# Optimization experiments

Hardware: AMD Instinct MI355X
Metric: run time of the kernel (lower is better)

Reference implementation:

```python
import jax, jax.numpy as jnp
import numpy as np
from jax import lax

D_MODEL, N_STATE, L_LEN = 1024, 64, 4096
DT_INIT = 0.1


def hippo_legs_matrix(N):
    # Standard HiPPO-LegS: A[n,k] = -sqrt(2n+1)sqrt(2k+1) if n>k, -(n+1) if n==k, 0 else
    n = np.arange(N, dtype=np.float32)
    r = np.sqrt(2.0 * n + 1.0)
    A = np.where(n[:, None] > n[None, :], r[:, None] * r[None, :], 0.0)
    A = -(A + np.diag(n + 1.0))
    B = r.copy()
    return jnp.asarray(A, jnp.float32), jnp.asarray(B, jnp.float32)


def setup_inputs() -> dict:
    key = jax.random.key(0)
    kB, kC = jax.random.split(key)
    A_ct, B_ref = hippo_legs_matrix(N_STATE)
    B0 = jnp.tile(B_ref[None, :], (D_MODEL, 1))
    B = B0 + 0.01 * jax.random.normal(kB, (D_MODEL, N_STATE), jnp.float32)
    C = jax.random.normal(kC, (D_MODEL, N_STATE), jnp.float32) * 0.1
    D = jnp.zeros((D_MODEL,), jnp.float32)
    log_dt = jnp.asarray(np.log(DT_INIT), jnp.float32)
    return {"A_ct": A_ct, "B": B, "C": C, "D": D, "log_dt": log_dt}


def reference(A_ct, B, C, D, log_dt):
    dt = jnp.exp(log_dt)
    N = A_ct.shape[0]
    I = jnp.eye(N, dtype=A_ct.dtype)
    M = I - (dt / 2.0) * A_ct          # (N,N)
    P = I + (dt / 2.0) * A_ct          # (N,N)
    A_bar = jnp.linalg.solve(M, P)     # (N,N)
    # B_bar[d] = M^{-1} (dt * B[d])  -> solve on transposed batch
    B_bar = jnp.linalg.solve(M, (dt * B).T).T  # (D,N)

    def step(x, _):
        # x: (D,N) state; emit readout then advance
        y = jnp.sum(C * x, axis=-1)    # (D,)
        return x @ A_bar.T, y

    _, ys = lax.scan(step, B_bar, None, length=L_LEN)  # ys: (L,D)
    K = ys.T                                           # (D,L)
    K = K.at[:, 0].add(D)
    return K[:, None, :]                                # (D,1,L)
```

## Files before the change

### kernel.cpp

```cpp
#include <hip/hip_runtime.h>
#include <math.h>


#define BPAD 72
#define ARR (64 * BPAD)

#define WS_BBAR   16
#define WS_SPL    65552
#define WS_MV     (WS_SPL + 12*8192)
#define WS_GT     (WS_MV + 4096)
#define WS_H      (WS_GT + 64*4096)
#define WS_W      (WS_H + 64*4096)
#define WS_X      (WS_W + 1024*4096)

using bf16x8 = __attribute__((ext_vector_type(8))) short;
using f32x4v = __attribute__((ext_vector_type(4))) float;
typedef unsigned short ushort_t;

__device__ __forceinline__ ushort_t f2bf(float x) {
  unsigned u = __builtin_bit_cast(unsigned, x);
  return (ushort_t)((u + 0x7FFFu + ((u >> 16) & 1u)) >> 16);
}
__device__ __forceinline__ float bfhi(float x) {
  unsigned u = __builtin_bit_cast(unsigned, x);
  unsigned r = (u + 0x7FFFu + ((u >> 16) & 1u)) & 0xFFFF0000u;
  return __builtin_bit_cast(float, r);
}
__device__ __forceinline__ ushort_t* usp(float* ws, int foff) {
  return (ushort_t*)(ws + foff);
}
__device__ __forceinline__ const ushort_t* uspc(const float* ws, int foff) {
  return (const ushort_t*)(ws + foff);
}

__device__ __forceinline__ void mm_frag(const ushort_t* __restrict__ Ah,
                                        const ushort_t* __restrict__ Al,
                                        const ushort_t* __restrict__ Bh,
                                        const ushort_t* __restrict__ Bl,
                                        int w, int lane, f32x4v acc[4]) {
  const int lm = lane & 15, quad = lane >> 4;
  const int ar = (16 * w + lm) * BPAD, ko = quad * 8;
#pragma unroll
  for (int nt = 0; nt < 4; ++nt) { acc[nt][0] = acc[nt][1] = acc[nt][2] = acc[nt][3] = 0.f; }
#pragma unroll
  for (int kc = 0; kc < 64; kc += 32) {
    const bf16x8 ahi = *(const bf16x8*)&Ah[ar + kc + ko];
    const bf16x8 alo = *(const bf16x8*)&Al[ar + kc + ko];
#pragma unroll
    for (int nt = 0; nt < 4; ++nt) {
      const int br = (16 * nt + lm) * BPAD + kc + ko;
      const bf16x8 bhi = *(const bf16x8*)&Bh[br];
      const bf16x8 blo = *(const bf16x8*)&Bl[br];
      acc[nt] = __builtin_amdgcn_mfma_f32_16x16x32_bf16(ahi, bhi, acc[nt], 0, 0, 0);
      acc[nt] = __builtin_amdgcn_mfma_f32_16x16x32_bf16(ahi, blo, acc[nt], 0, 0, 0);
      acc[nt] = __builtin_amdgcn_mfma_f32_16x16x32_bf16(alo, bhi, acc[nt], 0, 0, 0);
    }
  }
}

__device__ __forceinline__ void mm_frag16(const ushort_t* __restrict__ Ah,
                                          const ushort_t* __restrict__ Al,
                                          const ushort_t* __restrict__ Bh,
                                          const ushort_t* __restrict__ Bl,
                                          int mt, int nt, int lane, f32x4v& acc) {
  const int lm = lane & 15, quad = lane >> 4;
  const int ar = (16 * mt + lm) * BPAD, br = (16 * nt + lm) * BPAD, ko = quad * 8;
  acc[0] = acc[1] = acc[2] = acc[3] = 0.f;
#pragma unroll
  for (int kc = 0; kc < 64; kc += 32) {
    const bf16x8 ahi = *(const bf16x8*)&Ah[ar + kc + ko];
    const bf16x8 alo = *(const bf16x8*)&Al[ar + kc + ko];
    const bf16x8 bhi = *(const bf16x8*)&Bh[br + kc + ko];
    const bf16x8 blo = *(const bf16x8*)&Bl[br + kc + ko];
    acc = __builtin_amdgcn_mfma_f32_16x16x32_bf16(ahi, bhi, acc, 0, 0, 0);
    acc = __builtin_amdgcn_mfma_f32_16x16x32_bf16(ahi, blo, acc, 0, 0, 0);
    acc = __builtin_amdgcn_mfma_f32_16x16x32_bf16(alo, bhi, acc, 0, 0, 0);
  }
}

__device__ __forceinline__ void dstore_lds16(const f32x4v& acc,
                                             ushort_t* __restrict__ Ah, ushort_t* __restrict__ Al,
                                             ushort_t* __restrict__ Bth, ushort_t* __restrict__ Btl,
                                             int mt, int nt, int lane) {
  const int lm = lane & 15, quad = lane >> 4;
  const int m0 = 16 * mt + 4 * quad;
  const int n = 16 * nt + lm;
  ushort_t h[4], l[4];
#pragma unroll
  for (int reg = 0; reg < 4; ++reg) {
    const float x = acc[reg];
    h[reg] = f2bf(x); l[reg] = f2bf(x - bfhi(x));
    Ah[(m0 + reg) * BPAD + n] = h[reg];
    Al[(m0 + reg) * BPAD + n] = l[reg];
  }
  uint2 hp, lp;
  hp.x = (unsigned)h[0] | ((unsigned)h[1] << 16);
  hp.y = (unsigned)h[2] | ((unsigned)h[3] << 16);
  lp.x = (unsigned)l[0] | ((unsigned)l[1] << 16);
  lp.y = (unsigned)l[2] | ((unsigned)l[3] << 16);
  *(uint2*)&Bth[n * BPAD + m0] = hp;
  *(uint2*)&Btl[n * BPAD + m0] = lp;
}

__device__ __forceinline__ void dstore_A16(const f32x4v& acc,
                                           ushort_t* __restrict__ Ah, ushort_t* __restrict__ Al,
                                           int mt, int nt, int lane) {
  const int lm = lane & 15, quad = lane >> 4;
  const int m0 = 16 * mt + 4 * quad;
  const int n = 16 * nt + lm;
#pragma unroll
  for (int reg = 0; reg < 4; ++reg) {
    const float x = acc[reg];
    Ah[(m0 + reg) * BPAD + n] = f2bf(x);
    Al[(m0 + reg) * BPAD + n] = f2bf(x - bfhi(x));
  }
}

__device__ __forceinline__ void dstore_Bt16(const f32x4v& acc,
                                            ushort_t* __restrict__ Bth, ushort_t* __restrict__ Btl,
                                            int mt, int nt, int lane) {
  const int lm = lane & 15, quad = lane >> 4;
  const int m0 = 16 * mt + 4 * quad;
  const int n = 16 * nt + lm;
  ushort_t h[4], l[4];
#pragma unroll
  for (int reg = 0; reg < 4; ++reg) {
    const float x = acc[reg];
    h[reg] = f2bf(x); l[reg] = f2bf(x - bfhi(x));
  }
  uint2 hp, lp;
  hp.x = (unsigned)h[0] | ((unsigned)h[1] << 16);
  hp.y = (unsigned)h[2] | ((unsigned)h[3] << 16);
  lp.x = (unsigned)l[0] | ((unsigned)l[1] << 16);
  lp.y = (unsigned)l[2] | ((unsigned)l[3] << 16);
  *(uint2*)&Bth[n * BPAD + m0] = hp;
  *(uint2*)&Btl[n * BPAD + m0] = lp;
}

__device__ __forceinline__ void cp_l2w(const ushort_t* __restrict__ l,
                                       ushort_t* __restrict__ g, int tid, int NT) {
  for (int e = tid; e < 512; e += NT) {
    const int row = e >> 3, c8 = (e & 7) * 8;
    *(uint4*)&g[row * 64 + c8] = *(const uint4*)&l[row * BPAD + c8];
  }
}
__device__ __forceinline__ void cp_w2l(const ushort_t* __restrict__ g,
                                       ushort_t* __restrict__ l, int tid, int NT) {
  for (int e = tid; e < 512; e += NT) {
    const int row = e >> 3, c8 = (e & 7) * 8;
    *(uint4*)&l[row * BPAD + c8] = *(const uint4*)&g[row * 64 + c8];
  }
}

__device__ __forceinline__ void split_stage(const float* __restrict__ g,
                                            ushort_t* __restrict__ Ah,
                                            ushort_t* __restrict__ Al, int tid, int NT) {
  for (int flat = tid * 4; flat < 4096; flat += NT * 4) {
    const int row = flat >> 6, col = flat & 63;
    const float4 v = *(const float4*)&g[flat];
    ushort_t h0 = f2bf(v.x), h1 = f2bf(v.y), h2 = f2bf(v.z), h3 = f2bf(v.w);
    ushort_t l0 = f2bf(v.x - bfhi(v.x)), l1 = f2bf(v.y - bfhi(v.y));
    ushort_t l2 = f2bf(v.z - bfhi(v.z)), l3 = f2bf(v.w - bfhi(v.w));
    uint2 hp, lp;
    hp.x = (unsigned)h0 | ((unsigned)h1 << 16); hp.y = (unsigned)h2 | ((unsigned)h3 << 16);
    lp.x = (unsigned)l0 | ((unsigned)l1 << 16); lp.y = (unsigned)l2 | ((unsigned)l3 << 16);
    *(uint2*)&Ah[row * BPAD + col] = hp;
    *(uint2*)&Al[row * BPAD + col] = lp;
  }
}

__global__ __launch_bounds__(1024) void k_setup(const float* __restrict__ A,
                                                const float* __restrict__ logdt,
                                                float* __restrict__ ws) {
  __shared__ __align__(16) char SM[73728];
  float* Msh = (float*)SM;
  float* Tm  = (float*)(SM + 16640);
  float* tmpb = (float*)(SM + 33280);
  ushort_t* ping = (ushort_t*)SM;
  ushort_t* pong = (ushort_t*)(SM + 36864);
  const int tid = threadIdx.x;
  const int w = tid >> 6, lane = tid & 63;
  const int mt = w >> 2, nt = w & 3;
  const int NT = 1024;

  const float hdt = 0.5f * expf(logdt[0]);
  for (int idx = tid; idx < 4096; idx += NT) {
    const int i = idx >> 6, j = idx & 63;
    Msh[i * 65 + j] = ((i == j) ? 1.f : 0.f) - hdt * A[idx];
    Tm[i * 65 + j] = 0.f;
  }
  __syncthreads();
  if (tid < 64) Tm[tid * 65 + tid] = 1.0f / Msh[tid * 65 + tid];
  __syncthreads();
  for (int lb = 0; lb < 6; ++lb) {
    const int b = 1 << lb;
    const int E = 32 * b;
    for (int e = tid; e < E; e += NT) {
      const int rem = e & (b * b - 1);
      const int p = e >> (2 * lb);
      const int i = rem >> lb, j = rem & (b - 1);
      const int c0 = p << (lb + 1), r0 = c0 + b;
      float s = 0.f;
      for (int k = 0; k < b; ++k)
        s += Msh[(r0 + i) * 65 + c0 + k] * Tm[(c0 + k) * 65 + c0 + j];
      tmpb[e] = s;
    }
    __syncthreads();
    for (int e = tid; e < E; e += NT) {
      const int rem = e & (b * b - 1);
      const int p = e >> (2 * lb);
      const int i = rem >> lb, j = rem & (b - 1);
      const int c0 = p << (lb + 1), r0 = c0 + b;
      float s = 0.f;
      const float* tp = &tmpb[e - rem];
      for (int k = 0; k < b; ++k)
        s += Tm[(r0 + i) * 65 + r0 + k] * tp[k * b + j];
      Tm[(r0 + i) * 65 + c0 + j] = -s;
    }
    __syncthreads();
  }

  {
    ushort_t* MvH = usp(ws, WS_MV);
    ushort_t* MvL = usp(ws, WS_MV + 2048);
    float mv[4];
#pragma unroll
    for (int t4 = 0; t4 < 4; ++t4) {
      const int idx = tid + NT * t4;
      const float m = Tm[(idx >> 6) * 65 + (idx & 63)];
      mv[t4] = m;
      MvH[idx] = f2bf(m); MvL[idx] = f2bf(m - bfhi(m));
    }
    __syncthreads();
#pragma unroll
    for (int t4 = 0; t4 < 4; ++t4) {
      const int idx = tid + NT * t4;
      const int i = idx >> 6, j = idx & 63;
      const float v = 2.f * mv[t4] - ((i == j) ? 1.f : 0.f);
      const ushort_t h = f2bf(v), l2 = f2bf(v - bfhi(v));
      ping[0 * ARR + i * BPAD + j] = h; ping[1 * ARR + i * BPAD + j] = l2;
      ping[2 * ARR + j * BPAD + i] = h; ping[3 * ARR + j * BPAD + i] = l2;
    }
  }
  __syncthreads();
  cp_l2w(ping + 0 * ARR, usp(ws, WS_SPL + 0), tid, NT);
  cp_l2w(ping + 1 * ARR, usp(ws, WS_SPL + 2048), tid, NT);
  cp_l2w(ping + 2 * ARR, usp(ws, WS_SPL + 4096), tid, NT);
  cp_l2w(ping + 3 * ARR, usp(ws, WS_SPL + 6144), tid, NT);

  ushort_t* cur = ping;
  ushort_t* nxt = pong;
  for (int sj = 1; sj < 12; ++sj) {
    f32x4v acc;
    mm_frag16(cur, cur + ARR, cur + 2 * ARR, cur + 3 * ARR, mt, nt, lane, acc);
    dstore_lds16(acc, nxt, nxt + ARR, nxt + 2 * ARR, nxt + 3 * ARR, mt, nt, lane);
    __syncthreads();
    const int base = WS_SPL + sj * 8192;
    cp_l2w(nxt + 0 * ARR, usp(ws, base + 0), tid, NT);
    cp_l2w(nxt + 1 * ARR, usp(ws, base + 2048), tid, NT);
    cp_l2w(nxt + 2 * ARR, usp(ws, base + 4096), tid, NT);
    cp_l2w(nxt + 3 * ARR, usp(ws, base + 6144), tid, NT);
    ushort_t* t = cur; cur = nxt; nxt = t;
  }
}

__global__ __launch_bounds__(1024) void k_powers(const float* __restrict__ Bg,
                                                 const float* __restrict__ logdt,
                                                 float* __restrict__ ws) {
  __shared__ __align__(16) ushort_t SMp[4 * ARR];
  ushort_t* ca  = SMp;
  ushort_t* Bst = SMp + 2 * ARR;
  const int p = blockIdx.x, tid = threadIdx.x;
  const int w = tid >> 6, lane = tid & 63;
  const int mt = w >> 2, nt = w & 3;
  const int NT = 1024;

  if (p < 128) {
    const int chain = p >> 6, r = p & 63;
    ushort_t* dstH = usp(ws, (chain ? WS_H : WS_GT) + r * 4096);
    ushort_t* dstL = usp(ws, (chain ? WS_H : WS_GT) + r * 4096 + 2048);
    if (r == 0) {
      for (int idx = tid; idx < 4096; idx += NT) {
        const int i = idx >> 6, j = idx & 63;
        dstH[idx] = (i == j) ? (ushort_t)0x3F80 : (ushort_t)0;
        dstL[idx] = 0;
      }
      return;
    }
    const int j0 = __ffs(r) - 1;
    if (r == (1 << j0)) {
      const int sb = WS_SPL + (chain * 6 + j0) * 8192;
      const int src = chain ? sb : (sb + 4096);
      const uint4* sh = (const uint4*)uspc(ws, src);
      const uint4* sl = (const uint4*)uspc(ws, src + 2048);
      uint4* dh = (uint4*)dstH;
      uint4* dl = (uint4*)dstL;
      for (int e = tid; e < 512; e += NT) { dh[e] = sh[e]; dl[e] = sl[e]; }
      return;
    }
    {
      const int sb0 = WS_SPL + (chain * 6 + j0) * 8192;
      cp_w2l(uspc(ws, sb0 + 0), ca, tid, NT);
      cp_w2l(uspc(ws, sb0 + 2048), ca + ARR, tid, NT);
    }
    for (int j = j0 + 1; j < 6; ++j) {
      if ((r >> j) & 1) {
        __syncthreads();
        const int sb = WS_SPL + (chain * 6 + j) * 8192;
        cp_w2l(uspc(ws, sb + 4096), Bst, tid, NT);
        cp_w2l(uspc(ws, sb + 6144), Bst + ARR, tid, NT);
        __syncthreads();
        f32x4v acc;
        mm_frag16(ca, ca + ARR, Bst, Bst + ARR, mt, nt, lane, acc);
        __syncthreads();
        const bool last = ((r >> (j + 1)) == 0);
        if (last && chain == 0)
          dstore_Bt16(acc, Bst, Bst + ARR, mt, nt, lane);
        else
          dstore_A16(acc, ca, ca + ARR, mt, nt, lane);
      }
    }
    __syncthreads();
    if (chain == 0) { cp_l2w(Bst, dstH, tid, NT); cp_l2w(Bst + ARR, dstL, tid, NT); }
    else            { cp_l2w(ca, dstH, tid, NT);  cp_l2w(ca + ARR, dstL, tid, NT); }
  } else {
    const int d0 = (p - 128) * 64;
    const float dtv = expf(logdt[0]);
    split_stage(Bg + d0 * 64, ca, ca + ARR, tid, NT);
    cp_w2l(uspc(ws, WS_MV), Bst, tid, NT);
    cp_w2l(uspc(ws, WS_MV + 2048), Bst + ARR, tid, NT);
    __syncthreads();
    f32x4v acc;
    mm_frag16(ca, ca + ARR, Bst, Bst + ARR, mt, nt, lane, acc);
    const int lm = lane & 15, quad = lane >> 4;
    float* od = ws + WS_BBAR + d0 * 64;
#pragma unroll
    for (int reg = 0; reg < 4; ++reg)
      od[(16 * mt + 4 * quad + reg) * 64 + 16 * nt + lm] = dtv * acc[reg];
  }
}

__global__ __launch_bounds__(256) void k_expand(const float* __restrict__ Cg,
                                                float* __restrict__ ws) {
  __shared__ __align__(16) ushort_t SMe[4 * ARR];
  ushort_t* Asp = SMe;
  ushort_t* Bsp = SMe + 2 * ARR;
  const int p = blockIdx.x, tid = threadIdx.x;
  const int chain = p >> 10, rr = (p >> 4) & 63, dch = p & 15;
  const int w = tid >> 6, lane = tid & 63;
  const int d0 = dch * 64;

  split_stage(chain ? (ws + WS_BBAR + d0 * 64) : (Cg + d0 * 64), Asp, Asp + ARR, tid, 256);
  const int mb = (chain ? WS_H : WS_GT) + rr * 4096;
  cp_w2l(uspc(ws, mb + 0), Bsp, tid, 256);
  cp_w2l(uspc(ws, mb + 2048), Bsp + ARR, tid, 256);
  __syncthreads();

  f32x4v acc[4];
  mm_frag(Asp, Asp + ARR, Bsp, Bsp + ARR, w, lane, acc);

  const int lm = lane & 15, quad = lane >> 4;
  float* dst = ws + (chain ? WS_X : WS_W) + d0 * 4096 + rr * 64;
#pragma unroll
  for (int nt = 0; nt < 4; ++nt)
#pragma unroll
    for (int reg = 0; reg < 4; ++reg)
      dst[(16 * w + 4 * quad + reg) * 4096 + 16 * nt + lm] = acc[nt][reg];
}

__global__ __launch_bounds__(256) void k_contract(const float* __restrict__ Dg,
                                                  const float* __restrict__ ws,
                                                  float* __restrict__ out) {
  __shared__ __align__(16) ushort_t XhiL[64 * BPAD];
  __shared__ __align__(16) ushort_t XloL[64 * BPAD];
  __shared__ __align__(16) ushort_t WhiL[64 * BPAD];
  __shared__ __align__(16) ushort_t WloL[64 * BPAD];
  const int d = blockIdx.x, tid = threadIdx.x;
  const float* Wg = ws + WS_W + d * 4096;
  const float* Xg = ws + WS_X + d * 4096;

#pragma unroll
  for (int j = 0; j < 4; ++j) {
    const int flat = j * 1024 + tid * 4;
    const int row = flat >> 6, col = flat & 63;
    const float4 wv = *(const float4*)&Wg[flat];
    const float4 xv = *(const float4*)&Xg[flat];
    const int o = row * BPAD + col;
#pragma unroll
    for (int s = 0; s < 2; ++s) {
      const float4 v = s ? xv : wv;
      ushort_t h0 = f2bf(v.x), h1 = f2bf(v.y), h2 = f2bf(v.z), h3 = f2bf(v.w);
      ushort_t l0 = f2bf(v.x - bfhi(v.x)), l1 = f2bf(v.y - bfhi(v.y));
      ushort_t l2 = f2bf(v.z - bfhi(v.z)), l3 = f2bf(v.w - bfhi(v.w));
      uint2 hp, lp;
      hp.x = (unsigned)h0 | ((unsigned)h1 << 16); hp.y = (unsigned)h2 | ((unsigned)h3 << 16);
      lp.x = (unsigned)l0 | ((unsigned)l1 << 16); lp.y = (unsigned)l2 | ((unsigned)l3 << 16);
      *(uint2*)&(s ? XhiL : WhiL)[o] = hp;
      *(uint2*)&(s ? XloL : WloL)[o] = lp;
    }
  }
  __syncthreads();

  const int w = tid >> 6, lane = tid & 63;
  const int lm = lane & 15, quad = lane >> 4;
  const int qrow = 16 * w + lm;
  const int koff = quad * 8;

  f32x4v acc[4];
#pragma unroll
  for (int nt = 0; nt < 4; ++nt) { acc[nt][0] = 0.f; acc[nt][1] = 0.f; acc[nt][2] = 0.f; acc[nt][3] = 0.f; }

#pragma unroll
  for (int kc = 0; kc < 64; kc += 32) {
    const bf16x8 ahi = *(const bf16x8*)&XhiL[qrow * BPAD + kc + koff];
    const bf16x8 alo = *(const bf16x8*)&XloL[qrow * BPAD + kc + koff];
#pragma unroll
    for (int nt = 0; nt < 4; ++nt) {
      const int rrow = 16 * nt + lm;
      const bf16x8 bhi = *(const bf16x8*)&WhiL[rrow * BPAD + kc + koff];
      const bf16x8 blo = *(const bf16x8*)&WloL[rrow * BPAD + kc + koff];
      acc[nt] = __builtin_amdgcn_mfma_f32_16x16x32_bf16(ahi, bhi, acc[nt], 0, 0, 0);
      acc[nt] = __builtin_amdgcn_mfma_f32_16x16x32_bf16(ahi, blo, acc[nt], 0, 0, 0);
      acc[nt] = __builtin_amdgcn_mfma_f32_16x16x32_bf16(alo, bhi, acc[nt], 0, 0, 0);
    }
  }

  if (tid == 0) acc[0][0] += Dg[d];

  float* od = out + d * 4096;
#pragma unroll
  for (int nt = 0; nt < 4; ++nt) {
#pragma unroll
    for (int reg = 0; reg < 4; ++reg) {
      const int q = 16 * w + quad * 4 + reg;
      od[q * 64 + 16 * nt + lm] = acc[nt][reg];
    }
  }
}

extern "C" void kernel_launch(void* const* d_in, const int* in_sizes, int n_in,
                              void* d_out, int out_size, void* d_ws, size_t ws_size,
                              hipStream_t stream) {
  const float* A     = (const float*)d_in[0];
  const float* B     = (const float*)d_in[1];
  const float* C     = (const float*)d_in[2];
  const float* Dv    = (const float*)d_in[3];
  const float* logdt = (const float*)d_in[4];
  float* ws  = (float*)d_ws;
  float* out = (float*)d_out;

  hipLaunchKernelGGL(k_setup,    dim3(1),    dim3(1024), 0, stream, A, logdt, ws);
  hipLaunchKernelGGL(k_powers,   dim3(144),  dim3(1024), 0, stream, B, logdt, ws);
  hipLaunchKernelGGL(k_expand,   dim3(2048), dim3(256),  0, stream, C, ws);
  hipLaunchKernelGGL(k_contract, dim3(1024), dim3(256),  0, stream, Dv, ws, out);
}
```

Baseline: 119.6 us.

## Fuse setup and powers kernels by recomputing inverse and squarings per block

The single-block setup kernel, which computed the matrix inverse and repeated squarings, is merged into the 144-block powers kernel. Each block now recomputes the triangular inverse and only the squarings it needs, forming its power product locally. This removes one kernel launch and the serial single-block stage, along with the workspace round trip for the squared matrices. The cost is redundant inverse and squaring work in every block.

Result: faster. 114.9 us (-3.9%).

```diff
diff --git a/kernel.cpp b/kernel.cpp
--- a/kernel.cpp
+++ b/kernel.cpp
@@ -114,27 +114,6 @@
     Ah[(m0 + reg) * BPAD + n] = f2bf(x);
     Al[(m0 + reg) * BPAD + n] = f2bf(x - bfhi(x));
   }
-}
-
-__device__ __forceinline__ void dstore_Bt16(const f32x4v& acc,
-                                            ushort_t* __restrict__ Bth, ushort_t* __restrict__ Btl,
-                                            int mt, int nt, int lane) {
-  const int lm = lane & 15, quad = lane >> 4;
-  const int m0 = 16 * mt + 4 * quad;
-  const int n = 16 * nt + lm;
-  ushort_t h[4], l[4];
-#pragma unroll
-  for (int reg = 0; reg < 4; ++reg) {
-    const float x = acc[reg];
-    h[reg] = f2bf(x); l[reg] = f2bf(x - bfhi(x));
-  }
-  uint2 hp, lp;
-  hp.x = (unsigned)h[0] | ((unsigned)h[1] << 16);
-  hp.y = (unsigned)h[2] | ((unsigned)h[3] << 16);
-  lp.x = (unsigned)l[0] | ((unsigned)l[1] << 16);
-  lp.y = (unsigned)l[2] | ((unsigned)l[3] << 16);
-  *(uint2*)&Bth[n * BPAD + m0] = hp;
-  *(uint2*)&Btl[n * BPAD + m0] = lp;
 }
 
 __device__ __forceinline__ void cp_l2w(const ushort_t* __restrict__ l,
@@ -169,19 +148,35 @@
   }
 }
 
-__global__ __launch_bounds__(1024) void k_setup(const float* __restrict__ A,
-                                                const float* __restrict__ logdt,
-                                                float* __restrict__ ws) {
-  __shared__ __align__(16) char SM[73728];
-  float* Msh = (float*)SM;
-  float* Tm  = (float*)(SM + 16640);
+__global__ __launch_bounds__(1024) void k_prologue(const float* __restrict__ A,
+                                                   const float* __restrict__ Bg,
+                                                   const float* __restrict__ logdt,
+                                                   float* __restrict__ ws) {
+  __shared__ __align__(16) char SM[55296];
+  float* Msh  = (float*)SM;
+  float* Tm   = (float*)(SM + 16640);
   float* tmpb = (float*)(SM + 33280);
   ushort_t* ping = (ushort_t*)SM;
-  ushort_t* pong = (ushort_t*)(SM + 36864);
-  const int tid = threadIdx.x;
+  ushort_t* ca   = (ushort_t*)(SM + 36864);
+  const int p = blockIdx.x, tid = threadIdx.x;
   const int w = tid >> 6, lane = tid & 63;
-  const int mt = w >> 2, nt = w & 3;
+  const int mt = w >> 2, nt4 = w & 3;
+  const int lm = lane & 15, quad = lane >> 4;
   const int NT = 1024;
+
+  const int chain = (p < 128) ? (p >> 6) : 0;
+  const int rq = p & 63;
+
+  if (p < 128 && rq == 0) {
+    ushort_t* dstH = usp(ws, (chain ? WS_H : WS_GT));
+    ushort_t* dstL = dstH + 4096;
+    for (int idx = tid; idx < 4096; idx += NT) {
+      const int i = idx >> 6, j = idx & 63;
+      dstH[idx] = (i == j) ? (ushort_t)0x3F80 : (ushort_t)0;
+      dstL[idx] = 0;
+    }
+    return;
+  }
 
   const float hdt = 0.5f * expf(logdt[0]);
   for (int idx = tid; idx < 4096; idx += NT) {
@@ -197,9 +192,9 @@
     const int E = 32 * b;
     for (int e = tid; e < E; e += NT) {
       const int rem = e & (b * b - 1);
-      const int p = e >> (2 * lb);
+      const int pp = e >> (2 * lb);
       const int i = rem >> lb, j = rem & (b - 1);
-      const int c0 = p << (lb + 1), r0 = c0 + b;
+      const int c0 = pp << (lb + 1), r0 = c0 + b;
       float s = 0.f;
       for (int k = 0; k < b; ++k)
         s += Msh[(r0 + i) * 65 + c0 + k] * Tm[(c0 + k) * 65 + c0 + j];
@@ -208,9 +203,9 @@
     __syncthreads();
     for (int e = tid; e < E; e += NT) {
       const int rem = e & (b * b - 1);
-      const int p = e >> (2 * lb);
+      const int pp = e >> (2 * lb);
       const int i = rem >> lb, j = rem & (b - 1);
-      const int c0 = p << (lb + 1), r0 = c0 + b;
+      const int c0 = pp << (lb + 1), r0 = c0 + b;
       float s = 0.f;
       const float* tp = &tmpb[e - rem];
       for (int k = 0; k < b; ++k)
@@ -220,123 +215,116 @@
     __syncthreads();
   }
 
-  {
-    ushort_t* MvH = usp(ws, WS_MV);
-    ushort_t* MvL = usp(ws, WS_MV + 2048);
-    float mv[4];
-#pragma unroll
-    for (int t4 = 0; t4 < 4; ++t4) {
-      const int idx = tid + NT * t4;
-      const float m = Tm[(idx >> 6) * 65 + (idx & 63)];
-      mv[t4] = m;
-      MvH[idx] = f2bf(m); MvL[idx] = f2bf(m - bfhi(m));
-    }
-    __syncthreads();
+  float mv[4];
+#pragma unroll
+  for (int t4 = 0; t4 < 4; ++t4) {
+    const int idx = tid + NT * t4;
+    mv[t4] = Tm[(idx >> 6) * 65 + (idx & 63)];
+  }
+  __syncthreads();
+
+  if (p >= 128) {
+    const int d0 = (p - 128) * 64;
+    const float dtv = expf(logdt[0]);
+    ushort_t* Bh = ping;           ushort_t* Bl = ping + ARR;
+    ushort_t* Mh = ping + 2 * ARR; ushort_t* Ml = ping + 3 * ARR;
+    split_stage(Bg + d0 * 64, Bh, Bl, tid, NT);
 #pragma unroll
     for (int t4 = 0; t4 < 4; ++t4) {
       const int idx = tid + NT * t4;
       const int i = idx >> 6, j = idx & 63;
-      const float v = 2.f * mv[t4] - ((i == j) ? 1.f : 0.f);
-      const ushort_t h = f2bf(v), l2 = f2bf(v - bfhi(v));
-      ping[0 * ARR + i * BPAD + j] = h; ping[1 * ARR + i * BPAD + j] = l2;
-      ping[2 * ARR + j * BPAD + i] = h; ping[3 * ARR + j * BPAD + i] = l2;
-    }
-  }
-  __syncthreads();
-  cp_l2w(ping + 0 * ARR, usp(ws, WS_SPL + 0), tid, NT);
-  cp_l2w(ping + 1 * ARR, usp(ws, WS_SPL + 2048), tid, NT);
-  cp_l2w(ping + 2 * ARR, usp(ws, WS_SPL + 4096), tid, NT);
-  cp_l2w(ping + 3 * ARR, usp(ws, WS_SPL + 6144), tid, NT);
+      const float m = mv[t4];
+      Mh[i * BPAD + j] = f2bf(m);
+      Ml[i * BPAD + j] = f2bf(m - bfhi(m));
+    }
+    __syncthreads();
+    f32x4v acc;
+    mm_frag16(Bh, Bl, Mh, Ml, mt, nt4, lane, acc);
+    float* od = ws + WS_BBAR + d0 * 64;
+#pragma unroll
+    for (int reg = 0; reg < 4; ++reg)
+      od[(16 * mt + 4 * quad + reg) * 64 + 16 * nt4 + lm] = dtv * acc[reg];
+    return;
+  }
+
+  const int base6 = chain * 6;
+  const int j0   = (__ffs(rq) - 1) + base6;
+  const int jmax = (31 - __clz((unsigned)rq)) + base6;
+  const bool single = (j0 == jmax);
+
+#pragma unroll
+  for (int t4 = 0; t4 < 4; ++t4) {
+    const int idx = tid + NT * t4;
+    const int i = idx >> 6, j = idx & 63;
+    const float v = 2.f * mv[t4] - ((i == j) ? 1.f : 0.f);
+    const ushort_t h = f2bf(v), l2 = f2bf(v - bfhi(v));
+    ping[0 * ARR + i * BPAD + j] = h; ping[1 * ARR + i * BPAD + j] = l2;
+    ping[2 * ARR + j * BPAD + i] = h; ping[3 * ARR + j * BPAD + i] = l2;
+  }
+  __syncthreads();
 
   ushort_t* cur = ping;
-  ushort_t* nxt = pong;
-  for (int sj = 1; sj < 12; ++sj) {
-    f32x4v acc;
-    mm_frag16(cur, cur + ARR, cur + 2 * ARR, cur + 3 * ARR, mt, nt, lane, acc);
-    dstore_lds16(acc, nxt, nxt + ARR, nxt + 2 * ARR, nxt + 3 * ARR, mt, nt, lane);
+  ushort_t* cah = ca;
+  ushort_t* cal = ca + ARR;
+
+  for (int j = 0; j <= jmax; ++j) {
+    const bool isprod = (j > j0) && ((rq >> (j - base6)) & 1);
+    const bool dosq = (j < jmax);
+    if (j == j0 && !single) {
+      const int arr = tid >> 9, ei = tid & 511;
+      const int row = ei >> 3, c8 = (ei & 7) * 8;
+      *(uint4*)&ca[arr * ARR + row * BPAD + c8] =
+          *(const uint4*)&cur[arr * ARR + row * BPAD + c8];
+    }
+    f32x4v accp, accs;
+    if (isprod) mm_frag16(cah, cal, cur + 2 * ARR, cur + 3 * ARR, mt, nt4, lane, accp);
+    if (dosq)   mm_frag16(cur, cur + ARR, cur + 2 * ARR, cur + 3 * ARR, mt, nt4, lane, accs);
     __syncthreads();
-    const int base = WS_SPL + sj * 8192;
-    cp_l2w(nxt + 0 * ARR, usp(ws, base + 0), tid, NT);
-    cp_l2w(nxt + 1 * ARR, usp(ws, base + 2048), tid, NT);
-    cp_l2w(nxt + 2 * ARR, usp(ws, base + 4096), tid, NT);
-    cp_l2w(nxt + 3 * ARR, usp(ws, base + 6144), tid, NT);
-    ushort_t* t = cur; cur = nxt; nxt = t;
-  }
-}
-
-__global__ __launch_bounds__(1024) void k_powers(const float* __restrict__ Bg,
-                                                 const float* __restrict__ logdt,
-                                                 float* __restrict__ ws) {
-  __shared__ __align__(16) ushort_t SMp[4 * ARR];
-  ushort_t* ca  = SMp;
-  ushort_t* Bst = SMp + 2 * ARR;
-  const int p = blockIdx.x, tid = threadIdx.x;
-  const int w = tid >> 6, lane = tid & 63;
-  const int mt = w >> 2, nt = w & 3;
-  const int NT = 1024;
-
-  if (p < 128) {
-    const int chain = p >> 6, r = p & 63;
-    ushort_t* dstH = usp(ws, (chain ? WS_H : WS_GT) + r * 4096);
-    ushort_t* dstL = usp(ws, (chain ? WS_H : WS_GT) + r * 4096 + 2048);
-    if (r == 0) {
-      for (int idx = tid; idx < 4096; idx += NT) {
-        const int i = idx >> 6, j = idx & 63;
-        dstH[idx] = (i == j) ? (ushort_t)0x3F80 : (ushort_t)0;
-        dstL[idx] = 0;
+    if (isprod && !dosq) {
+      const int m0 = 16 * mt + 4 * quad, n = 16 * nt4 + lm;
+      ushort_t h[4], l[4];
+#pragma unroll
+      for (int reg = 0; reg < 4; ++reg) {
+        const float x = accp[reg];
+        h[reg] = f2bf(x); l[reg] = f2bf(x - bfhi(x));
+      }
+      if (chain == 0) {
+        ushort_t* dstH = usp(ws, WS_GT + rq * 4096);
+        ushort_t* dstL = dstH + 4096;
+        uint2 hp, lp;
+        hp.x = (unsigned)h[0] | ((unsigned)h[1] << 16);
+        hp.y = (unsigned)h[2] | ((unsigned)h[3] << 16);
+        lp.x = (unsigned)l[0] | ((unsigned)l[1] << 16);
+        lp.y = (unsigned)l[2] | ((unsigned)l[3] << 16);
+        *(uint2*)&dstH[n * 64 + m0] = hp;
+        *(uint2*)&dstL[n * 64 + m0] = lp;
+      } else {
+        ushort_t* dstH = usp(ws, WS_H + rq * 4096);
+        ushort_t* dstL = dstH + 4096;
+#pragma unroll
+        for (int reg = 0; reg < 4; ++reg) {
+          dstH[(m0 + reg) * 64 + n] = h[reg];
+          dstL[(m0 + reg) * 64 + n] = l[reg];
+        }
       }
       return;
     }
-    const int j0 = __ffs(r) - 1;
-    if (r == (1 << j0)) {
-      const int sb = WS_SPL + (chain * 6 + j0) * 8192;
-      const int src = chain ? sb : (sb + 4096);
-      const uint4* sh = (const uint4*)uspc(ws, src);
-      const uint4* sl = (const uint4*)uspc(ws, src + 2048);
-      uint4* dh = (uint4*)dstH;
-      uint4* dl = (uint4*)dstL;
-      for (int e = tid; e < 512; e += NT) { dh[e] = sh[e]; dl[e] = sl[e]; }
-      return;
-    }
-    {
-      const int sb0 = WS_SPL + (chain * 6 + j0) * 8192;
-      cp_w2l(uspc(ws, sb0 + 0), ca, tid, NT);
-      cp_w2l(uspc(ws, sb0 + 2048), ca + ARR, tid, NT);
-    }
-    for (int j = j0 + 1; j < 6; ++j) {
-      if ((r >> j) & 1) {
-        __syncthreads();
-        const int sb = WS_SPL + (chain * 6 + j) * 8192;
-        cp_w2l(uspc(ws, sb + 4096), Bst, tid, NT);
-        cp_w2l(uspc(ws, sb + 6144), Bst + ARR, tid, NT);
-        __syncthreads();
-        f32x4v acc;
-        mm_frag16(ca, ca + ARR, Bst, Bst + ARR, mt, nt, lane, acc);
-        __syncthreads();
-        const bool last = ((r >> (j + 1)) == 0);
-        if (last && chain == 0)
-          dstore_Bt16(acc, Bst, Bst + ARR, mt, nt, lane);
-        else
-          dstore_A16(acc, ca, ca + ARR, mt, nt, lane);
-      }
-    }
+    if (isprod) dstore_A16(accp, cah, cal, mt, nt4, lane);
+    if (dosq)   dstore_lds16(accs, cur, cur + ARR, cur + 2 * ARR, cur + 3 * ARR,
+                             mt, nt4, lane);
     __syncthreads();
-    if (chain == 0) { cp_l2w(Bst, dstH, tid, NT); cp_l2w(Bst + ARR, dstL, tid, NT); }
-    else            { cp_l2w(ca, dstH, tid, NT);  cp_l2w(ca + ARR, dstL, tid, NT); }
+  }
+
+  if (chain == 0) {
+    ushort_t* dstH = usp(ws, WS_GT + rq * 4096);
+    ushort_t* dstL = dstH + 4096;
+    cp_l2w(cur + 2 * ARR, dstH, tid, NT);
+    cp_l2w(cur + 3 * ARR, dstL, tid, NT);
   } else {
-    const int d0 = (p - 128) * 64;
-    const float dtv = expf(logdt[0]);
-    split_stage(Bg + d0 * 64, ca, ca + ARR, tid, NT);
-    cp_w2l(uspc(ws, WS_MV), Bst, tid, NT);
-    cp_w2l(uspc(ws, WS_MV + 2048), Bst + ARR, tid, NT);
-    __syncthreads();
-    f32x4v acc;
-    mm_frag16(ca, ca + ARR, Bst, Bst + ARR, mt, nt, lane, acc);
-    const int lm = lane & 15, quad = lane >> 4;
-    float* od = ws + WS_BBAR + d0 * 64;
-#pragma unroll
-    for (int reg = 0; reg < 4; ++reg)
-      od[(16 * mt + 4 * quad + reg) * 64 + 16 * nt + lm] = dtv * acc[reg];
+    ushort_t* dstH = usp(ws, WS_H + rq * 4096);
+    ushort_t* dstL = dstH + 4096;
+    cp_l2w(cur, dstH, tid, NT);
+    cp_l2w(cur + ARR, dstL, tid, NT);
   }
 }
 
@@ -449,8 +437,7 @@
   float* ws  = (float*)d_ws;
   float* out = (float*)d_out;
 
-  hipLaunchKernelGGL(k_setup,    dim3(1),    dim3(1024), 0, stream, A, logdt, ws);
-  hipLaunchKernelGGL(k_powers,   dim3(144),  dim3(1024), 0, stream, B, logdt, ws);
+  hipLaunchKernelGGL(k_prologue, dim3(144),  dim3(1024), 0, stream, A, B, logdt, ws);
   hipLaunchKernelGGL(k_expand,   dim3(2048), dim3(256),  0, stream, C, ws);
   hipLaunchKernelGGL(k_contract, dim3(1024), dim3(256),  0, stream, Dv, ws, out);
 }
```
